# Performance work log

Measured on AMD Instinct MI355X. Metric: run time of the kernel, lower is better.

## Reference

```python
import jax, jax.numpy as jnp
import numpy as np

N = 100000   # nodes
E = 1600000  # edges
F = 128      # num_features
H = 128      # embedding_size
C = 10       # num_classes
G = 64       # graphs in batch


def setup_inputs() -> dict:
    key = jax.random.key(0)
    ks = jax.random.split(key, 10)
    x = jax.random.normal(ks[0], (N, F), jnp.float32)
    edge_index = jax.random.randint(ks[1], (2, E), 0, N)
    batch_index = jnp.sort(jax.random.randint(ks[2], (N,), 0, G))
    glorot = lambda k, shape: jax.random.normal(k, shape, jnp.float32) / np.float32(np.sqrt(shape[0]))
    return {
        "x": x, "edge_index": edge_index, "batch_index": batch_index,
        "W0": glorot(ks[3], (F, H)), "b0": jnp.zeros((H,), jnp.float32),
        "W1": glorot(ks[4], (H, H)), "b1": jnp.zeros((H,), jnp.float32),
        "W2": glorot(ks[5], (H, H)), "b2": jnp.zeros((H,), jnp.float32),
        "W3": glorot(ks[6], (H, H)), "b3": jnp.zeros((H,), jnp.float32),
        "Wout": glorot(ks[7], (2 * H, C)), "bout": jnp.zeros((C,), jnp.float32),
    }


def gcn_conv(x, W, b, src, dst):
    """PyG GCNConv: self-loops + symmetric D^-1/2 (A+I) D^-1/2 normalization."""
    n = x.shape[0]
    # degree with self-loop: deg[i] = 1 + in-degree(i)
    deg = 1.0 + jax.ops.segment_sum(jnp.ones(dst.shape[0], x.dtype), dst, num_segments=n)
    dinv = jax.lax.rsqrt(deg)
    h = x @ W  # [N, H]
    norm = (dinv[src] * dinv[dst])[:, None]  # [E, 1]
    agg = jax.ops.segment_sum(h[src] * norm, dst, num_segments=n)  # scatter-add over edges
    agg = agg + h * (1.0 / deg)[:, None]  # self-loop contribution dinv[i]^2 * h[i]
    return agg + b


def reference(x, edge_index, batch_index, W0, b0, W1, b1, W2, b2, W3, b3, Wout, bout):
    src, dst = edge_index[0], edge_index[1]
    h = jnp.tanh(gcn_conv(x, W0, b0, src, dst))
    h = jnp.tanh(gcn_conv(h, W1, b1, src, dst))
    h = jnp.tanh(gcn_conv(h, W2, b2, src, dst))
    h = jnp.tanh(gcn_conv(h, W3, b3, src, dst))
    # global max pool + global mean pool over batch_index
    gmax = jax.ops.segment_max(h, batch_index, num_segments=G)
    cnt = jax.ops.segment_sum(jnp.ones((h.shape[0],), h.dtype), batch_index, num_segments=G)
    gmean = jax.ops.segment_sum(h, batch_index, num_segments=G) / jnp.maximum(cnt, 1.0)[:, None]
    pooled = jnp.concatenate([gmax, gmean], axis=1)  # [G, 2H]
    out = pooled @ Wout + bout  # [G, C]
    return out, pooled
```

## Files before the change

kernel.cpp:

```cpp
#include <hip/hip_runtime.h>
#include <hip/hip_fp16.h>
#include <cmath>

typedef __attribute__((ext_vector_type(8))) short short8;
typedef __attribute__((ext_vector_type(8))) unsigned short ushort8;
typedef __attribute__((ext_vector_type(8))) _Float16 f16x8;
typedef __attribute__((ext_vector_type(4))) float f32x4;

__device__ __forceinline__ unsigned pk_bf16(float a, float b) {
  unsigned r;
  asm("v_cvt_pk_bf16_f32 %0, %1, %2" : "=v"(r) : "v"(a), "v"(b));
  return r;
}

__device__ __forceinline__ float fast_tanh(float x) {
  float e2 = __expf(2.0f * x);
  return 1.0f - 2.0f * __builtin_amdgcn_rcpf(e2 + 1.0f);
}

#define FM_LO(A, U, W) \
  asm("v_fma_mix_f32 %0, %1, %2, %0 op_sel_hi:[1,0,0]" : "+v"(A) : "v"(U), "v"(W))
#define FM_HI(A, U, W) \
  asm("v_fma_mix_f32 %0, %1, %2, %0 op_sel:[1,0,0] op_sel_hi:[1,0,0]" : "+v"(A) : "v"(U), "v"(W))


__global__ __launch_bounds__(256) void count_k(const int* __restrict__ dst,
                                               int* __restrict__ cnt,
                                               int* __restrict__ epos, int E) {
  int e = blockIdx.x * 256 + threadIdx.x;
  if (e < E) epos[e] = atomicAdd(&cnt[dst[e]], 1);
}

__global__ __launch_bounds__(512) void scan_a(const int* __restrict__ cnt,
                                              int* __restrict__ rs,
                                              int* __restrict__ bsum,
                                              float* __restrict__ dinv,
                                              float* __restrict__ dinv2, int n) {
  __shared__ int s[512];
  int tid = threadIdx.x;
  int gid = blockIdx.x * 512 + tid;
  int v = (gid < n) ? cnt[gid] : 0;
  if (gid < n) {
    float deg = 1.0f + (float)v;
    dinv[gid] = rsqrtf(deg);
    dinv2[gid] = __builtin_amdgcn_rcpf(deg);
  }
  s[tid] = v;
  __syncthreads();
  for (int off = 1; off < 512; off <<= 1) {
    int t = (tid >= off) ? s[tid - off] : 0;
    __syncthreads();
    s[tid] += t;
    __syncthreads();
  }
  if (gid < n) rs[gid] = s[tid] - v;
  if (tid == 511) bsum[blockIdx.x] = s[511];
}

__global__ __launch_bounds__(256) void scan_b(const int* __restrict__ bsum,
                                              int* __restrict__ boff, int nb,
                                              const int* __restrict__ batch,
                                              int* __restrict__ gstart, int n,
                                              int G) {
  __shared__ int s[256];
  int tid = threadIdx.x;
  int v = (tid < nb) ? bsum[tid] : 0;
  s[tid] = v;
  __syncthreads();
  for (int off = 1; off < 256; off <<= 1) {
    int t = (tid >= off) ? s[tid - off] : 0;
    __syncthreads();
    s[tid] += t;
    __syncthreads();
  }
  if (tid < nb) boff[tid] = s[tid] - v;
  if (tid <= G) {
    int lo = 0, hi = n;
    while (lo < hi) {
      int mid = (lo + hi) >> 1;
      if (batch[mid] < tid) lo = mid + 1;
      else hi = mid;
    }
    gstart[tid] = lo;
  }
}

__global__ __launch_bounds__(512) void scan_c(const int* __restrict__ boff,
                                              int* __restrict__ rs, int n, int E) {
  int gid = blockIdx.x * 512 + threadIdx.x;
  if (gid < n) rs[gid] += boff[blockIdx.x];
  if (gid == 0) rs[n] = E;
}

__global__ __launch_bounds__(256) void fill_k(const int* __restrict__ src,
                                              const int* __restrict__ dst,
                                              const int* __restrict__ rs,
                                              const int* __restrict__ epos,
                                              const float* __restrict__ dinv,
                                              int2* __restrict__ edata, int E) {
  int e = blockIdx.x * 256 + threadIdx.x;
  if (e >= E) return;
  int s = src[e], d = dst[e];
  int pos = rs[d] + epos[e];
  int2 ed;
  ed.x = s;
  ed.y = __float_as_int(dinv[s] * dinv[d]);
  edata[pos] = ed;
}


__global__ __launch_bounds__(256) void wconv_all(const float* __restrict__ W0,
                                                 const float* __restrict__ W1,
                                                 const float* __restrict__ W2,
                                                 const float* __restrict__ W3,
                                                 unsigned short* __restrict__ Wt0Hi,
                                                 unsigned short* __restrict__ Wt0Lo,
                                                 unsigned short* __restrict__ WfHi,
                                                 unsigned short* __restrict__ WfLo) {
  int l = blockIdx.y;
  const float* W = (l == 0) ? W0 : (l == 1) ? W1 : (l == 2) ? W2 : W3;
  int idx = blockIdx.x * 256 + threadIdx.x;
  if (idx >= 8192) return;
  int n = idx & 127, k = (idx >> 7) * 2;
  float w0 = W[k * 128 + n], w1 = W[(k + 1) * 128 + n];
  if (l == 0) {
    unsigned h01 = pk_bf16(w0, w1);
    float hf0 = __uint_as_float(h01 << 16);
    float hf1 = __uint_as_float(h01 & 0xFFFF0000u);
    unsigned l01 = pk_bf16(w0 - hf0, w1 - hf1);
    *(unsigned*)&Wt0Hi[n * 128 + k] = h01;
    *(unsigned*)&Wt0Lo[n * 128 + k] = l01;
  } else {
    __half2 hh = __float22half2_rn(make_float2(w0, w1));
    float r0 = __low2float(hh), r1 = __high2float(hh);
    __half2 ll = __float22half2_rn(make_float2((w0 - r0) * 1024.0f,
                                               (w1 - r1) * 1024.0f));
    *(__half2*)&WfHi[(l - 1) * 16384 + n * 128 + k] = hh;
    *(__half2*)&WfLo[(l - 1) * 16384 + n * 128 + k] = ll;
  }
}


#define LDK 136

__global__ __launch_bounds__(256) void gemm_mfma(const float* __restrict__ A,
                                                 const unsigned short* __restrict__ WtHi,
                                                 const unsigned short* __restrict__ WtLo,
                                                 __half* __restrict__ O, int M) {
  __shared__ unsigned short sHi[128 * LDK];
  __shared__ unsigned short sLo[128 * LDK];
  int tid = threadIdx.x;
#pragma unroll
  for (int i = 0; i < 8; ++i) {
    int c = tid + i * 256;
    int n = c >> 4;
    int off = (c & 15) * 8;
    *(ushort8*)&sHi[n * LDK + off] = *(const ushort8*)&WtHi[c * 8];
    *(ushort8*)&sLo[n * LDK + off] = *(const ushort8*)&WtLo[c * 8];
  }
  __syncthreads();

  int wv = tid >> 6, lane = tid & 63;
  int r0 = blockIdx.x * 128 + wv * 32;
  int lrow = lane & 15, lk = (lane >> 4) * 8;

  f32x4 acc[2][8] = {};
#pragma unroll
  for (int kk = 0; kk < 4; ++kk) {
    int k0 = kk * 32 + lk;
    short8 ahi[2], alo[2];
#pragma unroll
    for (int fr = 0; fr < 2; ++fr) {
      int row = r0 + fr * 16 + lrow;
      row = row < M ? row : M - 1;
      const float* ap = &A[(size_t)row * 128 + k0];
      float4 a0 = *(const float4*)ap;
      float4 a1 = *(const float4*)(ap + 4);
      union { short8 v; unsigned u32[4]; } h_, l_;
#define SPLIT2(slot, x, y)                              \
      {                                                 \
        unsigned hh = pk_bf16((x), (y));                \
        h_.u32[slot] = hh;                              \
        float hf0 = __uint_as_float(hh << 16);          \
        float hf1 = __uint_as_float(hh & 0xFFFF0000u);  \
        l_.u32[slot] = pk_bf16((x) - hf0, (y) - hf1);   \
      }
      SPLIT2(0, a0.x, a0.y)
      SPLIT2(1, a0.z, a0.w)
      SPLIT2(2, a1.x, a1.y)
      SPLIT2(3, a1.z, a1.w)
#undef SPLIT2
      ahi[fr] = h_.v;
      alo[fr] = l_.v;
    }
#pragma unroll
    for (int c = 0; c < 8; ++c) {
      int bidx = (c * 16 + lrow) * LDK + k0;
      short8 bhi = *(const short8*)&sHi[bidx];
      short8 blo = *(const short8*)&sLo[bidx];
#pragma unroll
      for (int fr = 0; fr < 2; ++fr) {
        acc[fr][c] = __builtin_amdgcn_mfma_f32_16x16x32_bf16(ahi[fr], bhi, acc[fr][c], 0, 0, 0);
        acc[fr][c] = __builtin_amdgcn_mfma_f32_16x16x32_bf16(ahi[fr], blo, acc[fr][c], 0, 0, 0);
        acc[fr][c] = __builtin_amdgcn_mfma_f32_16x16x32_bf16(alo[fr], bhi, acc[fr][c], 0, 0, 0);
      }
    }
  }
#pragma unroll
  for (int fr = 0; fr < 2; ++fr) {
#pragma unroll
    for (int c = 0; c < 8; ++c) {
#pragma unroll
      for (int r = 0; r < 4; ++r) {
        int row = r0 + fr * 16 + (lane >> 4) * 4 + r;
        if (row < M)
          O[(size_t)row * 128 + c * 16 + (lane & 15)] = __float2half(acc[fr][c][r]);
      }
    }
  }
}


__global__ __launch_bounds__(256) void gemm_f16(const __half* __restrict__ Hf,
                                                const unsigned short* __restrict__ Whi,
                                                const unsigned short* __restrict__ Wlo,
                                                __half* __restrict__ O, int M) {
  __shared__ unsigned short sHi[128 * LDK];
  __shared__ unsigned short sLo[128 * LDK];
  int tid = threadIdx.x;
#pragma unroll
  for (int i = 0; i < 8; ++i) {
    int c = tid + i * 256;
    int n = c >> 4;
    int off = (c & 15) * 8;
    *(ushort8*)&sHi[n * LDK + off] = *(const ushort8*)&Whi[c * 8];
    *(ushort8*)&sLo[n * LDK + off] = *(const ushort8*)&Wlo[c * 8];
  }
  __syncthreads();

  int wv = tid >> 6, lane = tid & 63;
  int r0 = blockIdx.x * 128 + wv * 32;
  int lrow = lane & 15, lk = (lane >> 4) * 8;

  f32x4 acc[2][8] = {};
  f32x4 accL[2][8] = {};
#pragma unroll
  for (int kk = 0; kk < 4; ++kk) {
    int k0 = kk * 32 + lk;
    f16x8 a[2];
#pragma unroll
    for (int fr = 0; fr < 2; ++fr) {
      int row = r0 + fr * 16 + lrow;
      row = row < M ? row : M - 1;
      a[fr] = *(const f16x8*)&Hf[(size_t)row * 128 + k0];
    }
#pragma unroll
    for (int c = 0; c < 8; ++c) {
      int bidx = (c * 16 + lrow) * LDK + k0;
      f16x8 bhi = *(const f16x8*)&sHi[bidx];
      f16x8 blo = *(const f16x8*)&sLo[bidx];
#pragma unroll
      for (int fr = 0; fr < 2; ++fr) {
        acc[fr][c] = __builtin_amdgcn_mfma_f32_16x16x32_f16(a[fr], bhi, acc[fr][c], 0, 0, 0);
        accL[fr][c] = __builtin_amdgcn_mfma_f32_16x16x32_f16(a[fr], blo, accL[fr][c], 0, 0, 0);
      }
    }
  }
  const float ls = 1.0f / 1024.0f;
#pragma unroll
  for (int fr = 0; fr < 2; ++fr) {
#pragma unroll
    for (int c = 0; c < 8; ++c) {
#pragma unroll
      for (int r = 0; r < 4; ++r) {
        int row = r0 + fr * 16 + (lane >> 4) * 4 + r;
        if (row < M)
          O[(size_t)row * 128 + c * 16 + (lane & 15)] =
              __float2half(acc[fr][c][r] + accL[fr][c][r] * ls);
      }
    }
  }
}


template <bool FINAL>
__global__ __launch_bounds__(256) void gather_k(const __half* __restrict__ h,
                                                const int* __restrict__ rs,
                                                const int2* __restrict__ edata,
                                                const float* __restrict__ dinv2,
                                                const float* __restrict__ bias,
                                                __half* __restrict__ Hf,
                                                unsigned* __restrict__ OHi,
                                                unsigned* __restrict__ OLo, int N) {
  int wid = (int)((blockIdx.x * (size_t)blockDim.x + threadIdx.x) >> 6);
  if (wid >= N) return;
  int lane = threadIdx.x & 63;
  int grp = lane >> 4;
  int li = lane & 15;
  int s = rs[wid], e = rs[wid + 1];
  const uint4* hrow = (const uint4*)h;

  float ac[8] = {};
  int n16 = (e - s) >> 4;
  int base = s + grp;
#define ACC(U, W)                                        \
  {                                                      \
    FM_LO(ac[0], (U).x, (W)); FM_HI(ac[1], (U).x, (W));  \
    FM_LO(ac[2], (U).y, (W)); FM_HI(ac[3], (U).y, (W));  \
    FM_LO(ac[4], (U).z, (W)); FM_HI(ac[5], (U).z, (W));  \
    FM_LO(ac[6], (U).w, (W)); FM_HI(ac[7], (U).w, (W));  \
  }
  for (int it = 0; it < n16; ++it, base += 16) {
    int2 e0 = edata[base], e1 = edata[base + 4], e2 = edata[base + 8],
         e3 = edata[base + 12];
    float w0 = __int_as_float(e0.y), w1 = __int_as_float(e1.y),
          w2 = __int_as_float(e2.y), w3 = __int_as_float(e3.y);
    uint4 v0 = hrow[(size_t)e0.x * 16 + li];
    uint4 v1 = hrow[(size_t)e1.x * 16 + li];
    uint4 v2 = hrow[(size_t)e2.x * 16 + li];
    uint4 v3 = hrow[(size_t)e3.x * 16 + li];
    ACC(v0, w0) ACC(v1, w1) ACC(v2, w2) ACC(v3, w3)
  }
  for (int idx = base; idx < e; idx += 4) {
    int2 ed = edata[idx];
    float w = __int_as_float(ed.y);
    uint4 v = hrow[(size_t)ed.x * 16 + li];
    ACC(v, w)
  }
#undef ACC
#pragma unroll
  for (int j = 0; j < 8; ++j) {
    ac[j] += __shfl_xor(ac[j], 16);
    ac[j] += __shfl_xor(ac[j], 32);
  }

  float a0 = grp == 0 ? ac[0] : grp == 1 ? ac[2] : grp == 2 ? ac[4] : ac[6];
  float a1 = grp == 0 ? ac[1] : grp == 1 ? ac[3] : grp == 2 ? ac[5] : ac[7];

  float d2 = dinv2[wid];
  uint4 sv = hrow[(size_t)wid * 16 + li];
  unsigned su = grp == 0 ? sv.x : grp == 1 ? sv.y : grp == 2 ? sv.z : sv.w;
  float2 sj = __half22float2(*(__half2*)&su);
  float2 bj = *(const float2*)&bias[li * 8 + 2 * grp];
  float o0 = fast_tanh(a0 + sj.x * d2 + bj.x);
  float o1 = fast_tanh(a1 + sj.y * d2 + bj.y);

  if (FINAL) {
    unsigned hp = pk_bf16(o0, o1);
    float r0f = __uint_as_float(hp << 16);
    float r1f = __uint_as_float(hp & 0xFFFF0000u);
    unsigned lp = pk_bf16(o0 - r0f, o1 - r1f);
    unsigned idx = (unsigned)wid * 64 + li * 4 + grp;
    OHi[idx] = hp;
    OLo[idx] = lp;
  } else {
    __half2 hv = __float22half2_rn(make_float2(o0, o1));
    *(__half2*)&Hf[(size_t)wid * 128 + li * 8 + 2 * grp] = hv;
  }
}


#define CH 16

__global__ __launch_bounds__(128) void pool_partial(const unsigned short* __restrict__ Hi,
                                                    const unsigned short* __restrict__ Lo,
                                                    const int* __restrict__ gstart,
                                                    float* __restrict__ pmax,
                                                    float* __restrict__ psum) {
  int g = blockIdx.x, c = blockIdx.y, f = threadIdx.x;
  int s = gstart[g], e = gstart[g + 1];
  long long len = e - s;
  int cs = s + (int)(len * c / CH);
  int ce = s + (int)(len * (c + 1) / CH);
  float m = -INFINITY, sum = 0.f;
  for (int n = cs; n < ce; ++n) {
    unsigned hv = Hi[(size_t)n * 128 + f];
    unsigned lv = Lo[(size_t)n * 128 + f];
    float v = __uint_as_float(hv << 16) + __uint_as_float(lv << 16);
    m = fmaxf(m, v);
    sum += v;
  }
  pmax[((size_t)g * CH + c) * 128 + f] = m;
  psum[((size_t)g * CH + c) * 128 + f] = sum;
}

__global__ __launch_bounds__(128) void pool_head(const float* __restrict__ pmax,
                                                 const float* __restrict__ psum,
                                                 const int* __restrict__ gstart,
                                                 const float* __restrict__ Wout,
                                                 const float* __restrict__ bout,
                                                 float* __restrict__ out, int G) {
  __shared__ float pl[256];
  int g = blockIdx.x, f = threadIdx.x;
  float m = -INFINITY, s = 0.f;
  for (int c = 0; c < CH; ++c) {
    m = fmaxf(m, pmax[((size_t)g * CH + c) * 128 + f]);
    s += psum[((size_t)g * CH + c) * 128 + f];
  }
  int cnt = gstart[g + 1] - gstart[g];
  float mean = s / fmaxf((float)cnt, 1.0f);
  float* pooled = out + (size_t)G * 10;
  pooled[(size_t)g * 256 + f] = m;
  pooled[(size_t)g * 256 + 128 + f] = mean;
  pl[f] = m;
  pl[128 + f] = mean;
  __syncthreads();
  if (f < 10) {
    float acc = bout[f];
    for (int k = 0; k < 256; ++k) acc += pl[k] * Wout[k * 10 + f];
    out[(size_t)g * 10 + f] = acc;
  }
}


extern "C" void kernel_launch(void* const* d_in, const int* in_sizes, int n_in,
                              void* d_out, int out_size, void* d_ws, size_t ws_size,
                              hipStream_t stream) {
  const float* x = (const float*)d_in[0];
  const int* ei = (const int*)d_in[1];
  const int* batch = (const int*)d_in[2];
  const float* W[4] = {(const float*)d_in[3], (const float*)d_in[5],
                       (const float*)d_in[7], (const float*)d_in[9]};
  const float* Bz[4] = {(const float*)d_in[4], (const float*)d_in[6],
                        (const float*)d_in[8], (const float*)d_in[10]};
  const float* Wout = (const float*)d_in[11];
  const float* bout = (const float*)d_in[12];
  const int N = in_sizes[0] / 128;
  const int E = in_sizes[1] / 2;
  const int G = 64;
  const int* srcp = ei;
  const int* dstp = ei + E;
  float* out = (float*)d_out;

  char* wsb = (char*)d_ws;
  size_t off = 0;
  auto alloc = [&](size_t bytes) -> void* {
    void* p = wsb + off;
    off = (off + bytes + 255) & ~(size_t)255;
    return p;
  };
  __half* bufA = (__half*)alloc((size_t)N * 128 * 2);
  __half* Hf = (__half*)alloc((size_t)N * 128 * 2);
  unsigned* OHi = (unsigned*)alloc((size_t)N * 64 * 4);
  unsigned* OLo = (unsigned*)alloc((size_t)N * 64 * 4);
  int* cnt = (int*)alloc((size_t)N * 4);
  int* epos = (int*)alloc((size_t)E * 4);
  float* dinv = (float*)alloc((size_t)N * 4);
  float* dinv2 = (float*)alloc((size_t)N * 4);
  int* rs = (int*)alloc((size_t)(N + 1) * 4);
  int2* edata = (int2*)alloc((size_t)E * 8);
  int* bsum = (int*)alloc(4096);
  int* boff = (int*)alloc(4096);
  int* gstart = (int*)alloc(4096);
  float* pmax = (float*)alloc((size_t)G * CH * 128 * 4);
  float* psum = (float*)alloc((size_t)G * CH * 128 * 4);
  unsigned short* Wt0Hi = (unsigned short*)alloc(16384 * 2);
  unsigned short* Wt0Lo = (unsigned short*)alloc(16384 * 2);
  unsigned short* WfHi = (unsigned short*)alloc(3 * 16384 * 2);
  unsigned short* WfLo = (unsigned short*)alloc(3 * 16384 * 2);
  if (off > ws_size) return;

  hipMemsetAsync(cnt, 0, (size_t)N * 4, stream);

  count_k<<<(E + 255) / 256, 256, 0, stream>>>(dstp, cnt, epos, E);
  int nsb = (N + 511) / 512;
  scan_a<<<nsb, 512, 0, stream>>>(cnt, rs, bsum, dinv, dinv2, N);
  scan_b<<<1, 256, 0, stream>>>(bsum, boff, nsb, batch, gstart, N, G);
  scan_c<<<nsb, 512, 0, stream>>>(boff, rs, N, E);
  fill_k<<<(E + 255) / 256, 256, 0, stream>>>(srcp, dstp, rs, epos, dinv, edata, E);
  wconv_all<<<dim3(32, 4), 256, 0, stream>>>(W[0], W[1], W[2], W[3], Wt0Hi, Wt0Lo,
                                             WfHi, WfLo);

  int ggrid = (int)(((size_t)N * 64 + 255) / 256);
  for (int l = 0; l < 4; ++l) {
    if (l == 0)
      gemm_mfma<<<(N + 127) / 128, 256, 0, stream>>>(x, Wt0Hi, Wt0Lo, bufA, N);
    else
      gemm_f16<<<(N + 127) / 128, 256, 0, stream>>>(Hf, WfHi + (l - 1) * 16384,
                                                    WfLo + (l - 1) * 16384, bufA, N);
    if (l < 3)
      gather_k<false><<<ggrid, 256, 0, stream>>>(bufA, rs, edata, dinv2, Bz[l], Hf,
                                                 OHi, OLo, N);
    else
      gather_k<true><<<ggrid, 256, 0, stream>>>(bufA, rs, edata, dinv2, Bz[l], Hf,
                                                OHi, OLo, N);
  }

  pool_partial<<<dim3(G, CH), 128, 0, stream>>>((const unsigned short*)OHi,
                                                (const unsigned short*)OLo, gstart,
                                                pmax, psum);
  pool_head<<<G, 128, 0, stream>>>(pmax, psum, gstart, Wout, bout, out, G);
}
```

Baseline: 526.6 us.

## Merge preprocessing kernels, use decoupled-lookback scan, prefetch edges in gather

Fuses the edge-count kernel with the weight conversion kernel, and replaces the three-kernel scan with a single-pass decoupled-lookback scan that also computes the graph start offsets. It also writes edge data with nontemporal stores and software-pipelines the gather loop so the next edge batch is loaded ahead of the feature reads. The aim is fewer kernel launches and less dependent load latency in the gather. The lookback scan relies on blocks being scheduled in order, because later blocks spin on a status word that earlier blocks publish.

```diff
diff --git a/kernel.cpp b/kernel.cpp
--- a/kernel.cpp
+++ b/kernel.cpp
@@ -24,103 +24,22 @@
   asm("v_fma_mix_f32 %0, %1, %2, %0 op_sel:[1,0,0] op_sel_hi:[1,0,0]" : "+v"(A) : "v"(U), "v"(W))
 
 
-__global__ __launch_bounds__(256) void count_k(const int* __restrict__ dst,
-                                               int* __restrict__ cnt,
-                                               int* __restrict__ epos, int E) {
-  int e = blockIdx.x * 256 + threadIdx.x;
-  if (e < E) epos[e] = atomicAdd(&cnt[dst[e]], 1);
-}
-
-__global__ __launch_bounds__(512) void scan_a(const int* __restrict__ cnt,
-                                              int* __restrict__ rs,
-                                              int* __restrict__ bsum,
-                                              float* __restrict__ dinv,
-                                              float* __restrict__ dinv2, int n) {
-  __shared__ int s[512];
-  int tid = threadIdx.x;
-  int gid = blockIdx.x * 512 + tid;
-  int v = (gid < n) ? cnt[gid] : 0;
-  if (gid < n) {
-    float deg = 1.0f + (float)v;
-    dinv[gid] = rsqrtf(deg);
-    dinv2[gid] = __builtin_amdgcn_rcpf(deg);
-  }
-  s[tid] = v;
-  __syncthreads();
-  for (int off = 1; off < 512; off <<= 1) {
-    int t = (tid >= off) ? s[tid - off] : 0;
-    __syncthreads();
-    s[tid] += t;
-    __syncthreads();
-  }
-  if (gid < n) rs[gid] = s[tid] - v;
-  if (tid == 511) bsum[blockIdx.x] = s[511];
-}
-
-__global__ __launch_bounds__(256) void scan_b(const int* __restrict__ bsum,
-                                              int* __restrict__ boff, int nb,
-                                              const int* __restrict__ batch,
-                                              int* __restrict__ gstart, int n,
-                                              int G) {
-  __shared__ int s[256];
-  int tid = threadIdx.x;
-  int v = (tid < nb) ? bsum[tid] : 0;
-  s[tid] = v;
-  __syncthreads();
-  for (int off = 1; off < 256; off <<= 1) {
-    int t = (tid >= off) ? s[tid - off] : 0;
-    __syncthreads();
-    s[tid] += t;
-    __syncthreads();
-  }
-  if (tid < nb) boff[tid] = s[tid] - v;
-  if (tid <= G) {
-    int lo = 0, hi = n;
-    while (lo < hi) {
-      int mid = (lo + hi) >> 1;
-      if (batch[mid] < tid) lo = mid + 1;
-      else hi = mid;
-    }
-    gstart[tid] = lo;
-  }
-}
-
-__global__ __launch_bounds__(512) void scan_c(const int* __restrict__ boff,
-                                              int* __restrict__ rs, int n, int E) {
-  int gid = blockIdx.x * 512 + threadIdx.x;
-  if (gid < n) rs[gid] += boff[blockIdx.x];
-  if (gid == 0) rs[n] = E;
-}
-
-__global__ __launch_bounds__(256) void fill_k(const int* __restrict__ src,
-                                              const int* __restrict__ dst,
-                                              const int* __restrict__ rs,
-                                              const int* __restrict__ epos,
-                                              const float* __restrict__ dinv,
-                                              int2* __restrict__ edata, int E) {
-  int e = blockIdx.x * 256 + threadIdx.x;
-  if (e >= E) return;
-  int s = src[e], d = dst[e];
-  int pos = rs[d] + epos[e];
-  int2 ed;
-  ed.x = s;
-  ed.y = __float_as_int(dinv[s] * dinv[d]);
-  edata[pos] = ed;
-}
-
-
-__global__ __launch_bounds__(256) void wconv_all(const float* __restrict__ W0,
-                                                 const float* __restrict__ W1,
-                                                 const float* __restrict__ W2,
-                                                 const float* __restrict__ W3,
-                                                 unsigned short* __restrict__ Wt0Hi,
-                                                 unsigned short* __restrict__ Wt0Lo,
-                                                 unsigned short* __restrict__ WfHi,
-                                                 unsigned short* __restrict__ WfLo) {
-  int l = blockIdx.y;
+__global__ __launch_bounds__(256) void count_wconv(
+    const int* __restrict__ dst, int* __restrict__ cnt, int* __restrict__ epos,
+    int E, int nc, const float* __restrict__ W0, const float* __restrict__ W1,
+    const float* __restrict__ W2, const float* __restrict__ W3,
+    unsigned short* __restrict__ Wt0Hi, unsigned short* __restrict__ Wt0Lo,
+    unsigned short* __restrict__ WfHi, unsigned short* __restrict__ WfLo) {
+  int b = blockIdx.x;
+  if (b < nc) {
+    int e = b * 256 + threadIdx.x;
+    if (e < E) epos[e] = atomicAdd(&cnt[dst[e]], 1);
+    return;
+  }
+  int t = (b - nc) * 256 + threadIdx.x;
+  int l = t >> 13;
+  int idx = t & 8191;
   const float* W = (l == 0) ? W0 : (l == 1) ? W1 : (l == 2) ? W2 : W3;
-  int idx = blockIdx.x * 256 + threadIdx.x;
-  if (idx >= 8192) return;
   int n = idx & 127, k = (idx >> 7) * 2;
   float w0 = W[k * 128 + n], w1 = W[(k + 1) * 128 + n];
   if (l == 0) {
@@ -138,6 +57,90 @@
     *(__half2*)&WfHi[(l - 1) * 16384 + n * 128 + k] = hh;
     *(__half2*)&WfLo[(l - 1) * 16384 + n * 128 + k] = ll;
   }
+}
+
+
+__global__ __launch_bounds__(512) void scan_k(const int* __restrict__ cnt,
+                                              int* __restrict__ rs,
+                                              unsigned* __restrict__ status,
+                                              float* __restrict__ dinv,
+                                              float* __restrict__ dinv2,
+                                              const int* __restrict__ batch,
+                                              int* __restrict__ gstart, int n,
+                                              int E, int G) {
+  __shared__ int s[512];
+  __shared__ int sprev;
+  int b = blockIdx.x, tid = threadIdx.x;
+  int gid = b * 512 + tid;
+  int v = (gid < n) ? cnt[gid] : 0;
+  if (gid < n) {
+    float deg = 1.0f + (float)v;
+    dinv[gid] = rsqrtf(deg);
+    dinv2[gid] = __builtin_amdgcn_rcpf(deg);
+  }
+  s[tid] = v;
+  __syncthreads();
+  for (int off = 1; off < 512; off <<= 1) {
+    int t = (tid >= off) ? s[tid - off] : 0;
+    __syncthreads();
+    s[tid] += t;
+    __syncthreads();
+  }
+  int incl = s[tid];
+  int total = s[511];
+  if (tid == 0) {
+    if (b == 0) {
+      __hip_atomic_store(&status[0], (2u << 30) | (unsigned)total,
+                         __ATOMIC_RELAXED, __HIP_MEMORY_SCOPE_AGENT);
+      sprev = 0;
+    } else {
+      __hip_atomic_store(&status[b], (1u << 30) | (unsigned)total,
+                         __ATOMIC_RELAXED, __HIP_MEMORY_SCOPE_AGENT);
+      int sum = 0;
+      int p = b - 1;
+      while (true) {
+        unsigned st;
+        do {
+          st = __hip_atomic_load(&status[p], __ATOMIC_RELAXED,
+                                 __HIP_MEMORY_SCOPE_AGENT);
+        } while ((st >> 30) == 0);
+        sum += (int)(st & 0x3FFFFFFFu);
+        if ((st >> 30) == 2) break;
+        --p;
+      }
+      __hip_atomic_store(&status[b], (2u << 30) | (unsigned)(sum + total),
+                         __ATOMIC_RELAXED, __HIP_MEMORY_SCOPE_AGENT);
+      sprev = sum;
+    }
+  }
+  __syncthreads();
+  if (gid < n) rs[gid] = sprev + incl - v;
+  if (gid == n) rs[n] = E;
+  if (b == 0 && tid <= G) {
+    int lo = 0, hi = n;
+    while (lo < hi) {
+      int mid = (lo + hi) >> 1;
+      if (batch[mid] < tid) lo = mid + 1;
+      else hi = mid;
+    }
+    gstart[tid] = lo;
+  }
+}
+
+
+__global__ __launch_bounds__(256) void fill_k(const int* __restrict__ src,
+                                              const int* __restrict__ dst,
+                                              const int* __restrict__ rs,
+                                              const int* __restrict__ epos,
+                                              const float* __restrict__ dinv,
+                                              int2* __restrict__ edata, int E) {
+  int e = blockIdx.x * 256 + threadIdx.x;
+  if (e >= E) return;
+  int s = src[e], d = dst[e];
+  int pos = rs[d] + epos[e];
+  unsigned nw = __float_as_uint(dinv[s] * dinv[d]);
+  unsigned long long u = ((unsigned long long)nw << 32) | (unsigned)s;
+  __builtin_nontemporal_store(u, (unsigned long long*)&edata[pos]);
 }
 
 
@@ -310,16 +313,31 @@
     FM_LO(ac[4], (U).z, (W)); FM_HI(ac[5], (U).z, (W));  \
     FM_LO(ac[6], (U).w, (W)); FM_HI(ac[7], (U).w, (W));  \
   }
-  for (int it = 0; it < n16; ++it, base += 16) {
+  if (n16 > 0) {
     int2 e0 = edata[base], e1 = edata[base + 4], e2 = edata[base + 8],
          e3 = edata[base + 12];
-    float w0 = __int_as_float(e0.y), w1 = __int_as_float(e1.y),
-          w2 = __int_as_float(e2.y), w3 = __int_as_float(e3.y);
+    for (int it = 0; it < n16 - 1; ++it) {
+      int nb = base + 16;
+      uint4 v0 = hrow[(size_t)e0.x * 16 + li];
+      uint4 v1 = hrow[(size_t)e1.x * 16 + li];
+      uint4 v2 = hrow[(size_t)e2.x * 16 + li];
+      uint4 v3 = hrow[(size_t)e3.x * 16 + li];
+      int2 f0 = edata[nb], f1 = edata[nb + 4], f2 = edata[nb + 8],
+           f3 = edata[nb + 12];
+      float w0 = __int_as_float(e0.y), w1 = __int_as_float(e1.y),
+            w2 = __int_as_float(e2.y), w3 = __int_as_float(e3.y);
+      ACC(v0, w0) ACC(v1, w1) ACC(v2, w2) ACC(v3, w3)
+      e0 = f0; e1 = f1; e2 = f2; e3 = f3;
+      base = nb;
+    }
     uint4 v0 = hrow[(size_t)e0.x * 16 + li];
     uint4 v1 = hrow[(size_t)e1.x * 16 + li];
     uint4 v2 = hrow[(size_t)e2.x * 16 + li];
     uint4 v3 = hrow[(size_t)e3.x * 16 + li];
+    float w0 = __int_as_float(e0.y), w1 = __int_as_float(e1.y),
+          w2 = __int_as_float(e2.y), w3 = __int_as_float(e3.y);
     ACC(v0, w0) ACC(v1, w1) ACC(v2, w2) ACC(v3, w3)
+    base += 16;
   }
   for (int idx = base; idx < e; idx += 4) {
     int2 ed = edata[idx];
@@ -350,9 +368,9 @@
     float r0f = __uint_as_float(hp << 16);
     float r1f = __uint_as_float(hp & 0xFFFF0000u);
     unsigned lp = pk_bf16(o0 - r0f, o1 - r1f);
-    unsigned idx = (unsigned)wid * 64 + li * 4 + grp;
-    OHi[idx] = hp;
-    OLo[idx] = lp;
+    unsigned oidx = (unsigned)wid * 64 + li * 4 + grp;
+    OHi[oidx] = hp;
+    OLo[oidx] = lp;
   } else {
     __half2 hv = __float22half2_rn(make_float2(o0, o1));
     *(__half2*)&Hf[(size_t)wid * 128 + li * 8 + 2 * grp] = hv;
@@ -443,14 +461,16 @@
   __half* Hf = (__half*)alloc((size_t)N * 128 * 2);
   unsigned* OHi = (unsigned*)alloc((size_t)N * 64 * 4);
   unsigned* OLo = (unsigned*)alloc((size_t)N * 64 * 4);
+  size_t cnt_off = off;
   int* cnt = (int*)alloc((size_t)N * 4);
+  int nsb = (N + 511) / 512;
+  unsigned* status = (unsigned*)alloc((size_t)nsb * 4);
+  size_t cnt_span = off - cnt_off;
   int* epos = (int*)alloc((size_t)E * 4);
   float* dinv = (float*)alloc((size_t)N * 4);
   float* dinv2 = (float*)alloc((size_t)N * 4);
   int* rs = (int*)alloc((size_t)(N + 1) * 4);
   int2* edata = (int2*)alloc((size_t)E * 8);
-  int* bsum = (int*)alloc(4096);
-  int* boff = (int*)alloc(4096);
   int* gstart = (int*)alloc(4096);
   float* pmax = (float*)alloc((size_t)G * CH * 128 * 4);
   float* psum = (float*)alloc((size_t)G * CH * 128 * 4);
@@ -460,16 +480,14 @@
   unsigned short* WfLo = (unsigned short*)alloc(3 * 16384 * 2);
   if (off > ws_size) return;
 
-  hipMemsetAsync(cnt, 0, (size_t)N * 4, stream);
-
-  count_k<<<(E + 255) / 256, 256, 0, stream>>>(dstp, cnt, epos, E);
-  int nsb = (N + 511) / 512;
-  scan_a<<<nsb, 512, 0, stream>>>(cnt, rs, bsum, dinv, dinv2, N);
-  scan_b<<<1, 256, 0, stream>>>(bsum, boff, nsb, batch, gstart, N, G);
-  scan_c<<<nsb, 512, 0, stream>>>(boff, rs, N, E);
+  hipMemsetAsync(wsb + cnt_off, 0, cnt_span, stream);
+
+  int nc = (E + 255) / 256;
+  count_wconv<<<nc + 128, 256, 0, stream>>>(dstp, cnt, epos, E, nc, W[0], W[1],
+                                            W[2], W[3], Wt0Hi, Wt0Lo, WfHi, WfLo);
+  scan_k<<<nsb, 512, 0, stream>>>(cnt, rs, status, dinv, dinv2, batch, gstart, N,
+                                  E, G);
   fill_k<<<(E + 255) / 256, 256, 0, stream>>>(srcp, dstp, rs, epos, dinv, edata, E);
-  wconv_all<<<dim3(32, 4), 256, 0, stream>>>(W[0], W[1], W[2], W[3], Wt0Hi, Wt0Lo,
-                                             WfHi, WfLo);
 
   int ggrid = (int)(((size_t)N * 64 + 255) / 256);
   for (int l = 0; l < 4; ++l) {
```

Result: slower. 551.3 us (+4.7%).

## Fuse count and weight conversion, predicate gather tail, drop split-precision final output

Applied to the files above, without the earlier changes.

Merges the edge-count kernel and the weight-conversion kernel into one launch by splitting block ranges. The gather loop is rewritten so partial tail groups are handled with predicated, zero-weighted loads inside the main 16-edge loop, and edge data is fetched with nontemporal 64-bit loads. The final layer now writes fp16 like the earlier layers instead of a bf16 hi/lo pair, so pooling reads half the bytes. That last step trades output precision in the pooled features for less memory traffic and removes one template variant.

```diff
diff --git a/kernel.cpp b/kernel.cpp
--- a/kernel.cpp
+++ b/kernel.cpp
@@ -24,103 +24,22 @@
   asm("v_fma_mix_f32 %0, %1, %2, %0 op_sel:[1,0,0] op_sel_hi:[1,0,0]" : "+v"(A) : "v"(U), "v"(W))
 
 
-__global__ __launch_bounds__(256) void count_k(const int* __restrict__ dst,
-                                               int* __restrict__ cnt,
-                                               int* __restrict__ epos, int E) {
-  int e = blockIdx.x * 256 + threadIdx.x;
-  if (e < E) epos[e] = atomicAdd(&cnt[dst[e]], 1);
-}
-
-__global__ __launch_bounds__(512) void scan_a(const int* __restrict__ cnt,
-                                              int* __restrict__ rs,
-                                              int* __restrict__ bsum,
-                                              float* __restrict__ dinv,
-                                              float* __restrict__ dinv2, int n) {
-  __shared__ int s[512];
-  int tid = threadIdx.x;
-  int gid = blockIdx.x * 512 + tid;
-  int v = (gid < n) ? cnt[gid] : 0;
-  if (gid < n) {
-    float deg = 1.0f + (float)v;
-    dinv[gid] = rsqrtf(deg);
-    dinv2[gid] = __builtin_amdgcn_rcpf(deg);
-  }
-  s[tid] = v;
-  __syncthreads();
-  for (int off = 1; off < 512; off <<= 1) {
-    int t = (tid >= off) ? s[tid - off] : 0;
-    __syncthreads();
-    s[tid] += t;
-    __syncthreads();
-  }
-  if (gid < n) rs[gid] = s[tid] - v;
-  if (tid == 511) bsum[blockIdx.x] = s[511];
-}
-
-__global__ __launch_bounds__(256) void scan_b(const int* __restrict__ bsum,
-                                              int* __restrict__ boff, int nb,
-                                              const int* __restrict__ batch,
-                                              int* __restrict__ gstart, int n,
-                                              int G) {
-  __shared__ int s[256];
-  int tid = threadIdx.x;
-  int v = (tid < nb) ? bsum[tid] : 0;
-  s[tid] = v;
-  __syncthreads();
-  for (int off = 1; off < 256; off <<= 1) {
-    int t = (tid >= off) ? s[tid - off] : 0;
-    __syncthreads();
-    s[tid] += t;
-    __syncthreads();
-  }
-  if (tid < nb) boff[tid] = s[tid] - v;
-  if (tid <= G) {
-    int lo = 0, hi = n;
-    while (lo < hi) {
-      int mid = (lo + hi) >> 1;
-      if (batch[mid] < tid) lo = mid + 1;
-      else hi = mid;
-    }
-    gstart[tid] = lo;
-  }
-}
-
-__global__ __launch_bounds__(512) void scan_c(const int* __restrict__ boff,
-                                              int* __restrict__ rs, int n, int E) {
-  int gid = blockIdx.x * 512 + threadIdx.x;
-  if (gid < n) rs[gid] += boff[blockIdx.x];
-  if (gid == 0) rs[n] = E;
-}
-
-__global__ __launch_bounds__(256) void fill_k(const int* __restrict__ src,
-                                              const int* __restrict__ dst,
-                                              const int* __restrict__ rs,
-                                              const int* __restrict__ epos,
-                                              const float* __restrict__ dinv,
-                                              int2* __restrict__ edata, int E) {
-  int e = blockIdx.x * 256 + threadIdx.x;
-  if (e >= E) return;
-  int s = src[e], d = dst[e];
-  int pos = rs[d] + epos[e];
-  int2 ed;
-  ed.x = s;
-  ed.y = __float_as_int(dinv[s] * dinv[d]);
-  edata[pos] = ed;
-}
-
-
-__global__ __launch_bounds__(256) void wconv_all(const float* __restrict__ W0,
-                                                 const float* __restrict__ W1,
-                                                 const float* __restrict__ W2,
-                                                 const float* __restrict__ W3,
-                                                 unsigned short* __restrict__ Wt0Hi,
-                                                 unsigned short* __restrict__ Wt0Lo,
-                                                 unsigned short* __restrict__ WfHi,
-                                                 unsigned short* __restrict__ WfLo) {
-  int l = blockIdx.y;
+__global__ __launch_bounds__(256) void count_wconv(
+    const int* __restrict__ dst, int* __restrict__ cnt, int* __restrict__ epos,
+    int E, int nc, const float* __restrict__ W0, const float* __restrict__ W1,
+    const float* __restrict__ W2, const float* __restrict__ W3,
+    unsigned short* __restrict__ Wt0Hi, unsigned short* __restrict__ Wt0Lo,
+    unsigned short* __restrict__ WfHi, unsigned short* __restrict__ WfLo) {
+  int b = blockIdx.x;
+  if (b < nc) {
+    int e = b * 256 + threadIdx.x;
+    if (e < E) epos[e] = atomicAdd(&cnt[dst[e]], 1);
+    return;
+  }
+  int t = (b - nc) * 256 + threadIdx.x;
+  int l = t >> 13;
+  int idx = t & 8191;
   const float* W = (l == 0) ? W0 : (l == 1) ? W1 : (l == 2) ? W2 : W3;
-  int idx = blockIdx.x * 256 + threadIdx.x;
-  if (idx >= 8192) return;
   int n = idx & 127, k = (idx >> 7) * 2;
   float w0 = W[k * 128 + n], w1 = W[(k + 1) * 128 + n];
   if (l == 0) {
@@ -138,6 +57,85 @@
     *(__half2*)&WfHi[(l - 1) * 16384 + n * 128 + k] = hh;
     *(__half2*)&WfLo[(l - 1) * 16384 + n * 128 + k] = ll;
   }
+}
+
+
+__global__ __launch_bounds__(512) void scan_a(const int* __restrict__ cnt,
+                                              int* __restrict__ rs,
+                                              int* __restrict__ bsum,
+                                              float* __restrict__ dinv,
+                                              float* __restrict__ dinv2, int n) {
+  __shared__ int s[512];
+  int tid = threadIdx.x;
+  int gid = blockIdx.x * 512 + tid;
+  int v = (gid < n) ? cnt[gid] : 0;
+  if (gid < n) {
+    float deg = 1.0f + (float)v;
+    dinv[gid] = rsqrtf(deg);
+    dinv2[gid] = __builtin_amdgcn_rcpf(deg);
+  }
+  s[tid] = v;
+  __syncthreads();
+  for (int off = 1; off < 512; off <<= 1) {
+    int t = (tid >= off) ? s[tid - off] : 0;
+    __syncthreads();
+    s[tid] += t;
+    __syncthreads();
+  }
+  if (gid < n) rs[gid] = s[tid] - v;
+  if (tid == 511) bsum[blockIdx.x] = s[511];
+}
+
+__global__ __launch_bounds__(256) void scan_b(const int* __restrict__ bsum,
+                                              int* __restrict__ boff, int nb,
+                                              const int* __restrict__ batch,
+                                              int* __restrict__ gstart, int n,
+                                              int G) {
+  __shared__ int s[256];
+  int tid = threadIdx.x;
+  int v = (tid < nb) ? bsum[tid] : 0;
+  s[tid] = v;
+  __syncthreads();
+  for (int off = 1; off < 256; off <<= 1) {
+    int t = (tid >= off) ? s[tid - off] : 0;
+    __syncthreads();
+    s[tid] += t;
+    __syncthreads();
+  }
+  if (tid < nb) boff[tid] = s[tid] - v;
+  if (tid <= G) {
+    int lo = 0, hi = n;
+    while (lo < hi) {
+      int mid = (lo + hi) >> 1;
+      if (batch[mid] < tid) lo = mid + 1;
+      else hi = mid;
+    }
+    gstart[tid] = lo;
+  }
+}
+
+__global__ __launch_bounds__(512) void scan_c(const int* __restrict__ boff,
+                                              int* __restrict__ rs, int n, int E) {
+  int gid = blockIdx.x * 512 + threadIdx.x;
+  if (gid < n) rs[gid] += boff[blockIdx.x];
+  if (gid == 0) rs[n] = E;
+}
+
+
+__global__ __launch_bounds__(256) void fill_k(const int* __restrict__ src,
+                                              const int* __restrict__ dst,
+                                              const int* __restrict__ rs,
+                                              const int* __restrict__ epos,
+                                              const float* __restrict__ dinv,
+                                              int2* __restrict__ edata, int E) {
+  int e = blockIdx.x * 256 + threadIdx.x;
+  if (e >= E) return;
+  int s = src[e], d = dst[e];
+  int pos = rs[d] + epos[e];
+  int2 ed;
+  ed.x = s;
+  ed.y = __float_as_int(dinv[s] * dinv[d]);
+  edata[pos] = ed;
 }
 
 
@@ -283,15 +281,12 @@
 }
 
 
-template <bool FINAL>
 __global__ __launch_bounds__(256) void gather_k(const __half* __restrict__ h,
                                                 const int* __restrict__ rs,
                                                 const int2* __restrict__ edata,
                                                 const float* __restrict__ dinv2,
                                                 const float* __restrict__ bias,
-                                                __half* __restrict__ Hf,
-                                                unsigned* __restrict__ OHi,
-                                                unsigned* __restrict__ OLo, int N) {
+                                                __half* __restrict__ Hf, int N) {
   int wid = (int)((blockIdx.x * (size_t)blockDim.x + threadIdx.x) >> 6);
   if (wid >= N) return;
   int lane = threadIdx.x & 63;
@@ -299,9 +294,10 @@
   int li = lane & 15;
   int s = rs[wid], e = rs[wid + 1];
   const uint4* hrow = (const uint4*)h;
+  const unsigned long long* ed64 = (const unsigned long long*)edata;
 
   float ac[8] = {};
-  int n16 = (e - s) >> 4;
+  int niter = (e - s + 15) >> 4;
   int base = s + grp;
 #define ACC(U, W)                                        \
   {                                                      \
@@ -310,22 +306,25 @@
     FM_LO(ac[4], (U).z, (W)); FM_HI(ac[5], (U).z, (W));  \
     FM_LO(ac[6], (U).w, (W)); FM_HI(ac[7], (U).w, (W));  \
   }
-  for (int it = 0; it < n16; ++it, base += 16) {
-    int2 e0 = edata[base], e1 = edata[base + 4], e2 = edata[base + 8],
-         e3 = edata[base + 12];
-    float w0 = __int_as_float(e0.y), w1 = __int_as_float(e1.y),
-          w2 = __int_as_float(e2.y), w3 = __int_as_float(e3.y);
-    uint4 v0 = hrow[(size_t)e0.x * 16 + li];
-    uint4 v1 = hrow[(size_t)e1.x * 16 + li];
-    uint4 v2 = hrow[(size_t)e2.x * 16 + li];
-    uint4 v3 = hrow[(size_t)e3.x * 16 + li];
+  for (int it = 0; it < niter; ++it, base += 16) {
+    int p0 = base, p1 = base + 4, p2 = base + 8, p3 = base + 12;
+    int c0 = p0 < e ? p0 : s, c1 = p1 < e ? p1 : s;
+    int c2 = p2 < e ? p2 : s, c3 = p3 < e ? p3 : s;
+    unsigned long long u0 = __builtin_nontemporal_load(&ed64[c0]);
+    unsigned long long u1 = __builtin_nontemporal_load(&ed64[c1]);
+    unsigned long long u2 = __builtin_nontemporal_load(&ed64[c2]);
+    unsigned long long u3 = __builtin_nontemporal_load(&ed64[c3]);
+    unsigned i0 = (unsigned)u0, i1 = (unsigned)u1;
+    unsigned i2 = (unsigned)u2, i3 = (unsigned)u3;
+    float w0 = p0 < e ? __uint_as_float((unsigned)(u0 >> 32)) : 0.0f;
+    float w1 = p1 < e ? __uint_as_float((unsigned)(u1 >> 32)) : 0.0f;
+    float w2 = p2 < e ? __uint_as_float((unsigned)(u2 >> 32)) : 0.0f;
+    float w3 = p3 < e ? __uint_as_float((unsigned)(u3 >> 32)) : 0.0f;
+    uint4 v0 = hrow[(size_t)i0 * 16 + li];
+    uint4 v1 = hrow[(size_t)i1 * 16 + li];
+    uint4 v2 = hrow[(size_t)i2 * 16 + li];
+    uint4 v3 = hrow[(size_t)i3 * 16 + li];
     ACC(v0, w0) ACC(v1, w1) ACC(v2, w2) ACC(v3, w3)
-  }
-  for (int idx = base; idx < e; idx += 4) {
-    int2 ed = edata[idx];
-    float w = __int_as_float(ed.y);
-    uint4 v = hrow[(size_t)ed.x * 16 + li];
-    ACC(v, w)
   }
 #undef ACC
 #pragma unroll
@@ -345,25 +344,14 @@
   float o0 = fast_tanh(a0 + sj.x * d2 + bj.x);
   float o1 = fast_tanh(a1 + sj.y * d2 + bj.y);
 
-  if (FINAL) {
-    unsigned hp = pk_bf16(o0, o1);
-    float r0f = __uint_as_float(hp << 16);
-    float r1f = __uint_as_float(hp & 0xFFFF0000u);
-    unsigned lp = pk_bf16(o0 - r0f, o1 - r1f);
-    unsigned idx = (unsigned)wid * 64 + li * 4 + grp;
-    OHi[idx] = hp;
-    OLo[idx] = lp;
-  } else {
-    __half2 hv = __float22half2_rn(make_float2(o0, o1));
-    *(__half2*)&Hf[(size_t)wid * 128 + li * 8 + 2 * grp] = hv;
-  }
+  __half2 hv = __float22half2_rn(make_float2(o0, o1));
+  *(__half2*)&Hf[(size_t)wid * 128 + li * 8 + 2 * grp] = hv;
 }
 
 
 #define CH 16
 
-__global__ __launch_bounds__(128) void pool_partial(const unsigned short* __restrict__ Hi,
-                                                    const unsigned short* __restrict__ Lo,
+__global__ __launch_bounds__(128) void pool_partial(const __half* __restrict__ Hf,
                                                     const int* __restrict__ gstart,
                                                     float* __restrict__ pmax,
                                                     float* __restrict__ psum) {
@@ -374,9 +362,7 @@
   int ce = s + (int)(len * (c + 1) / CH);
   float m = -INFINITY, sum = 0.f;
   for (int n = cs; n < ce; ++n) {
-    unsigned hv = Hi[(size_t)n * 128 + f];
-    unsigned lv = Lo[(size_t)n * 128 + f];
-    float v = __uint_as_float(hv << 16) + __uint_as_float(lv << 16);
+    float v = __half2float(Hf[(size_t)n * 128 + f]);
     m = fmaxf(m, v);
     sum += v;
   }
@@ -441,9 +427,9 @@
   };
   __half* bufA = (__half*)alloc((size_t)N * 128 * 2);
   __half* Hf = (__half*)alloc((size_t)N * 128 * 2);
-  unsigned* OHi = (unsigned*)alloc((size_t)N * 64 * 4);
-  unsigned* OLo = (unsigned*)alloc((size_t)N * 64 * 4);
+  size_t cnt_off = off;
   int* cnt = (int*)alloc((size_t)N * 4);
+  size_t cnt_span = off - cnt_off;
   int* epos = (int*)alloc((size_t)E * 4);
   float* dinv = (float*)alloc((size_t)N * 4);
   float* dinv2 = (float*)alloc((size_t)N * 4);
@@ -460,16 +446,16 @@
   unsigned short* WfLo = (unsigned short*)alloc(3 * 16384 * 2);
   if (off > ws_size) return;
 
-  hipMemsetAsync(cnt, 0, (size_t)N * 4, stream);
-
-  count_k<<<(E + 255) / 256, 256, 0, stream>>>(dstp, cnt, epos, E);
+  hipMemsetAsync(wsb + cnt_off, 0, cnt_span, stream);
+
+  int nc = (E + 255) / 256;
+  count_wconv<<<nc + 128, 256, 0, stream>>>(dstp, cnt, epos, E, nc, W[0], W[1],
+                                            W[2], W[3], Wt0Hi, Wt0Lo, WfHi, WfLo);
   int nsb = (N + 511) / 512;
   scan_a<<<nsb, 512, 0, stream>>>(cnt, rs, bsum, dinv, dinv2, N);
   scan_b<<<1, 256, 0, stream>>>(bsum, boff, nsb, batch, gstart, N, G);
   scan_c<<<nsb, 512, 0, stream>>>(boff, rs, N, E);
   fill_k<<<(E + 255) / 256, 256, 0, stream>>>(srcp, dstp, rs, epos, dinv, edata, E);
-  wconv_all<<<dim3(32, 4), 256, 0, stream>>>(W[0], W[1], W[2], W[3], Wt0Hi, Wt0Lo,
-                                             WfHi, WfLo);
 
   int ggrid = (int)(((size_t)N * 64 + 255) / 256);
   for (int l = 0; l < 4; ++l) {
@@ -478,16 +464,9 @@
     else
       gemm_f16<<<(N + 127) / 128, 256, 0, stream>>>(Hf, WfHi + (l - 1) * 16384,
                                                     WfLo + (l - 1) * 16384, bufA, N);
-    if (l < 3)
-      gather_k<false><<<ggrid, 256, 0, stream>>>(bufA, rs, edata, dinv2, Bz[l], Hf,
-                                                 OHi, OLo, N);
-    else
-      gather_k<true><<<ggrid, 256, 0, stream>>>(bufA, rs, edata, dinv2, Bz[l], Hf,
-                                                OHi, OLo, N);
-  }
-
-  pool_partial<<<dim3(G, CH), 128, 0, stream>>>((const unsigned short*)OHi,
-                                                (const unsigned short*)OLo, gstart,
-                                                pmax, psum);
+    gather_k<<<ggrid, 256, 0, stream>>>(bufA, rs, edata, dinv2, Bz[l], Hf, N);
+  }
+
+  pool_partial<<<dim3(G, CH), 128, 0, stream>>>(Hf, gstart, pmax, psum);
   pool_head<<<G, 128, 0, stream>>>(pmax, psum, gstart, Wout, bout, out, G);
 }
```

Measured after the change: 516.3 us. 1.02x faster.
